# Kernel tuning notes

Hardware: AMD Instinct MI355X
Metric: run time of the kernel (lower is better)

The kernel has to match this reference:

```python
import jax, jax.numpy as jnp
import numpy as np

B, L, C, P, LEVEL, K = 32, 1024, 128, 96, 3, 5
N_NODES = 2 ** (LEVEL + 1) - 1  # 15 CIL blocks in the tree (preorder: node, even-subtree, odd-subtree)
SQRT2 = np.float32(np.sqrt(2.0))


def haar_last(x):
    # Haar wavelet transform along last axis (power-of-2 length), iterative form of the torch recursion:
    # result = [h_final, g_deepest, ..., g_first]
    outs = []
    h = x
    while h.shape[-1] > 1:
        e, o = h[..., ::2], h[..., 1::2]
        outs.append((e - o) / SQRT2)
        h = (e + o) / SQRT2
    return jnp.concatenate([h] + outs[::-1], axis=-1)


def conv1d(x, w, b):
    # x: [B, C, L], w: [O, I, K], b: [O]
    y = jax.lax.conv_general_dilated(x, w, (1,), 'VALID', dimension_numbers=('NCH', 'OIH', 'NCH'))
    return y + b[None, :, None]


def causal_conv_block(x, w1, b1, w2, b2):
    # ReplicationPad1d((K-1, K-1)) -> Conv1d(K) -> LeakyReLU(0.01) -> Conv1d(K) -> Tanh; length preserved
    xp = jnp.pad(x, ((0, 0), (0, 0), (K - 1, K - 1)), mode='edge')
    y = conv1d(xp, w1, b1)
    y = jnp.where(y > 0, y, 0.01 * y)
    return jnp.tanh(conv1d(y, w2, b2))


def cil_block(x, bw1, bb1, bw2, bb2):
    # x: [B, L, C]; bw*: [4, C, C, K] ordered (modules_even, modules_odd, interactor_even, interactor_odd)
    xe = x[:, ::2].transpose(0, 2, 1)   # [B, C, L/2]
    xo = x[:, 1::2].transpose(0, 2, 1)
    ccb = lambda i, z: causal_conv_block(z, bw1[i], bb1[i], bw2[i], bb2[i])
    xet = xe * jnp.exp(ccb(0, xo))
    xot = xo * jnp.exp(ccb(1, xe))
    xeu = xet + ccb(2, xot)
    xou = xot - ccb(3, xet)
    return xeu.transpose(0, 2, 1), xou.transpose(0, 2, 1)


def zip_up(e, o):
    # interleave even/odd halves along the time axis (equal lengths since L is a power of 2)
    b, l, c = e.shape
    return jnp.stack([e, o], axis=2).reshape(b, 2 * l, c)


def _forward(x_enc, mask, fc1_w, fc2_w, ln_g, ln_b, w1, b1, w2, b2, proj_w):
    denom = jnp.sum((mask == 1).astype(x_enc.dtype), axis=1)                 # [B, C]
    means = jax.lax.stop_gradient(jnp.sum(x_enc, axis=1) / denom)[:, None]   # [B, 1, C] (detached)
    x = x_enc - means
    x = jnp.where(mask == 0, 0.0, x)
    stdev = jax.lax.stop_gradient(jnp.sqrt(jnp.sum(x * x, axis=1) / denom + 1e-5))[:, None]
    x = x / stdev
    # haar channel gating block (per-channel haar over time, FC gate, LayerNorm over L)
    freq = haar_last(x.transpose(0, 2, 1))                                   # [B, C, L]
    lr = jax.nn.sigmoid(jax.nn.relu(freq @ fc1_w.T) @ fc2_w.T)               # [B, C, L]
    mu = lr.mean(-1, keepdims=True)
    var = ((lr - mu) ** 2).mean(-1, keepdims=True)                           # biased, as torch LayerNorm
    lr = (lr - mu) / jnp.sqrt(var + 1e-6) * ln_g + ln_b
    x = x * lr.transpose(0, 2, 1)
    # sinusoidal position encoding (pe_hidden_size == C, even)
    num_ts = C // 2
    inc = np.float32(np.log(10000.0) / max(num_ts - 1, 1))
    inv = jnp.exp(jnp.arange(num_ts, dtype=jnp.float32) * -inc)
    st = jnp.arange(L, dtype=jnp.float32)[:, None] * inv[None, :]
    pe = jnp.concatenate([jnp.sin(st), jnp.cos(st)], axis=1)[None]           # [1, L, C]
    x = x + pe
    # recursive CILN tree; node params indexed in call order (node, even-subtree, odd-subtree)
    counter = [0]
    def tree(z, level):
        i = counter[0]; counter[0] += 1
        e, o = cil_block(z, w1[i], b1[i], w2[i], b2[i])
        if level == 0:
            return zip_up(e, o)
        return zip_up(tree(e, level - 1), tree(o, level - 1))
    dec = tree(x, LEVEL) + x
    dec = jnp.einsum('pl,blc->bpc', proj_w, dec)                             # Conv1d(L, L+P, k=1, bias=False) over time dim
    dec = dec * stdev + means
    # forward(): cat(zeros_like(x_enc), dec)[:, -P:, :3] == dec[:, -P:, :3]
    return dec[:, -P:, :3]


def setup_inputs():
    key = jax.random.key(0)
    ks = jax.random.split(key, 8)
    s = 0.05
    return {
        'x_enc': jax.random.normal(ks[0], (B, L, C), jnp.float32),
        'mask': jnp.ones((B, L, C), jnp.float32),
        'fc1_w': jax.random.normal(ks[1], (2 * L, L), jnp.float32) * s,
        'fc2_w': jax.random.normal(ks[2], (L, 2 * L), jnp.float32) * s,
        'ln_g': jnp.ones((L,), jnp.float32),
        'ln_b': jnp.zeros((L,), jnp.float32),
        'w1': jax.random.normal(ks[3], (N_NODES, 4, C, C, K), jnp.float32) * s,
        'b1': jax.random.normal(ks[4], (N_NODES, 4, C), jnp.float32) * s,
        'w2': jax.random.normal(ks[5], (N_NODES, 4, C, C, K), jnp.float32) * s,
        'b2': jax.random.normal(ks[6], (N_NODES, 4, C), jnp.float32) * s,
        'proj_w': jax.random.normal(ks[7], (L + P, L), jnp.float32) * s,
    }


def reference(x_enc, mask, fc1_w, fc2_w, ln_g, ln_b, w1, b1, w2, b2, proj_w):
    return _forward(x_enc, mask, fc1_w, fc2_w, ln_g, ln_b, w1, b1, w2, b2, proj_w)
```

## Files before the change

### kernel.cpp

```cpp
#include <hip/hip_runtime.h>

namespace {

constexpr int NB = 32, NL = 1024, NC = 128, NP = 96, KW = 5;
constexpr float INV_SQRT2 = 0.70710678118654752440f;
constexpr size_t SEG = (size_t)NB * NC;
constexpr int CT = 64;

typedef unsigned short u16;
typedef __attribute__((ext_vector_type(4))) u16 u16x4;
typedef __attribute__((ext_vector_type(8))) u16 u16x8;
typedef __attribute__((ext_vector_type(8))) short short8;
typedef __attribute__((ext_vector_type(4))) float f32x4;

__device__ inline u16 f2bf(float f) {
  unsigned u = __float_as_uint(f);
  u += 0x7fff + ((u >> 16) & 1);
  return (u16)(u >> 16);
}

__device__ inline float ftanh(float x) {
  float e = __expf(2.f * x);
  return 1.f - 2.f / (e + 1.f);
}

__device__ __forceinline__ void glds16(const void* g, void* l) {
  __builtin_amdgcn_global_load_lds(
      (const __attribute__((address_space(1))) unsigned*)g,
      (__attribute__((address_space(3))) unsigned*)l, 16, 0, 0);
}

__global__ void stats1(const float* __restrict__ x, const float* __restrict__ mask,
                       float* __restrict__ part) {
  int b = blockIdx.x, s = blockIdx.y;
  int tid = threadIdx.x;
  int c = tid & 127, lh = tid >> 7;
  const float* xb = x + (size_t)b * NL * NC;
  const float* mb = mask + (size_t)b * NL * NC;
  float s_all = 0.f, d1 = 0.f, sm = 0.f, sm2 = 0.f, cnz = 0.f;
#pragma unroll 4
  for (int i = 0; i < 32; ++i) {
    int l = s * 64 + lh + 2 * i;
    float v = xb[(size_t)l * NC + c];
    float m = mb[(size_t)l * NC + c];
    s_all += v;
    d1 += (m == 1.f) ? 1.f : 0.f;
    bool nz = (m != 0.f);
    float vm = nz ? v : 0.f;
    sm += vm;
    sm2 += vm * v;
    cnz += nz ? 1.f : 0.f;
  }
  __shared__ float red[5][256];
  red[0][tid] = s_all; red[1][tid] = d1; red[2][tid] = sm;
  red[3][tid] = sm2;   red[4][tid] = cnz;
  __syncthreads();
  if (lh == 0) {
    float* pp = part + ((size_t)(b * 16 + s) * 5) * NC + c;
#pragma unroll
    for (int q = 0; q < 5; ++q) pp[q * NC] = red[q][c] + red[q][c + 128];
  }
}

__global__ void stats2(const float* __restrict__ part, float* __restrict__ means,
                       float* __restrict__ stdev) {
  int b = blockIdx.x, c = threadIdx.x;
  float s_all = 0.f, d1 = 0.f, sm = 0.f, sm2 = 0.f, cnz = 0.f;
  for (int s = 0; s < 16; ++s) {
    const float* pp = part + ((size_t)(b * 16 + s) * 5) * NC + c;
    s_all += pp[0];
    d1    += pp[NC];
    sm    += pp[2 * NC];
    sm2   += pp[3 * NC];
    cnz   += pp[4 * NC];
  }
  float mn = s_all / d1;
  float varsum = sm2 - 2.f * mn * sm + mn * mn * cnz;
  means[b * NC + c] = mn;
  stdev[b * NC + c] = sqrtf(varsum / d1 + 1e-5f);
}

__global__ void norm_transpose(const float* __restrict__ x, const float* __restrict__ mask,
                               const float* __restrict__ means, const float* __restrict__ stdev,
                               float* __restrict__ xt) {
  __shared__ float tile[32][33];
  int b = blockIdx.x;
  int l0 = blockIdx.y * 32;
  int c0 = blockIdx.z * 32;
  int tx = threadIdx.x;
  int ty = threadIdx.y;
  for (int i = ty; i < 32; i += 8) {
    int l = l0 + i, c = c0 + tx;
    float v = x[((size_t)b * NL + l) * NC + c];
    float m = mask[((size_t)b * NL + l) * NC + c];
    float val = (m == 0.f) ? 0.f : (v - means[b * NC + c]);
    tile[i][tx] = val / stdev[b * NC + c];
  }
  __syncthreads();
  for (int i = ty; i < 32; i += 8) {
    xt[((size_t)b * NC + c0 + i) * NL + l0 + tx] = tile[tx][i];
  }
}

__global__ void haar_kernel(const float* __restrict__ xt, u16* __restrict__ freqb) {
  int row = blockIdx.x;
  __shared__ float h[1024], t2[512];
  const float* src = xt + (size_t)row * NL;
  u16* dst = freqb + (size_t)row * NL;
  for (int i = threadIdx.x; i < 1024; i += 256) h[i] = src[i];
  __syncthreads();
  int n = 1024;
  while (n > 1) {
    int half = n >> 1;
    for (int i = threadIdx.x; i < half; i += 256) {
      float e = h[2 * i], o = h[2 * i + 1];
      dst[half + i] = f2bf((e - o) * INV_SQRT2);
      t2[i] = (e + o) * INV_SQRT2;
    }
    __syncthreads();
    for (int i = threadIdx.x; i < half; i += 256) h[i] = t2[i];
    __syncthreads();
    n = half;
  }
  if (threadIdx.x == 0) dst[0] = f2bf(h[0]);
}

__global__ void cvt2(const float* __restrict__ in1, const float* __restrict__ in2,
                     u16* __restrict__ o1, u16* __restrict__ o2, int n4) {
  int i = blockIdx.x * 256 + threadIdx.x;
  const float* in = (i < n4) ? in1 : in2;
  u16* op = (i < n4) ? o1 : o2;
  int j = (i < n4) ? i : i - n4;
  if (j < n4) {
    const float4 v = *reinterpret_cast<const float4*>(in + (size_t)j * 4);
    u16x4 o;
    o.x = f2bf(v.x); o.y = f2bf(v.y); o.z = f2bf(v.z); o.w = f2bf(v.w);
    *reinterpret_cast<u16x4*>(op + (size_t)j * 4) = o;
  }
}

__global__ void pack2(const float* __restrict__ w1, const float* __restrict__ w2,
                      u16* __restrict__ wp1, u16* __restrict__ wp2) {
  int idx = blockIdx.x * 256 + threadIdx.x;
  const int NW = 60 * 128 * 128;
  const float* w = (idx < NW) ? w1 : w2;
  u16* wp = (idx < NW) ? wp1 : wp2;
  int j = (idx < NW) ? idx : idx - NW;
  if (j < NW) {
    int ci = j & 127;
    int co = (j >> 7) & 127;
    int n = j >> 14;
    const float* src = w + (size_t)j * 5;
    size_t base = (size_t)n * (5 * 128 * 128) + (size_t)co * 128 + ci;
#pragma unroll
    for (int k = 0; k < 5; ++k)
      wp[base + (size_t)k * 16384] = f2bf(src[k]);
  }
}

__global__ __launch_bounds__(256) void gemm_n128(const u16* __restrict__ A,
                                                 const u16* __restrict__ Bw,
                                                 u16* __restrict__ Cb,
                                                 int M, int N, int K, int CM, int CN) {
  __shared__ __align__(16) char sAB[256 * 128];
  int GX = gridDim.x;
  int h = blockIdx.y * GX + blockIdx.x;
  int xcd = h & 7, loc = h >> 3;
  int lm = loc / CN, ln = loc - lm * CN;
  int cnch = GX / CN;
  int m0 = ((xcd / cnch) * CM + lm) * 128;
  int n0 = ((xcd % cnch) * CN + ln) * 128;
  int tid = threadIdx.x;
  int lane = tid & 63, wv = tid >> 6;
  int wm = (wv >> 1) * 64, wn = (wv & 1) * 64;
  int lg = lane >> 4, l15 = lane & 15;

  const u16* srcb[8];
  int swo[8];
#pragma unroll
  for (int pass = 0; pass < 8; ++pass) {
    int o = pass * 4096 + tid * 16;
    int cb = o & 127;
    int row;
    if (pass < 4) {
      row = o >> 7;
      srcb[pass] = A + (size_t)(m0 + row) * K + (cb >> 1);
    } else {
      int rb = (o - 16384) >> 7;
      row = 128 + rb;
      srcb[pass] = Bw + (size_t)(n0 + rb) * K + (cb >> 1);
    }
    swo[pass] = row * 128 + (cb ^ ((row & 7) << 4));
  }

  f32x4 zero = {0.f, 0.f, 0.f, 0.f};
  f32x4 acc[4][4];
#pragma unroll
  for (int i = 0; i < 4; ++i)
#pragma unroll
    for (int j = 0; j < 4; ++j) acc[i][j] = zero;

  u16x8 st[8];
#pragma unroll
  for (int p = 0; p < 8; ++p) st[p] = *(const u16x8*)(srcb[p]);

  for (int k0 = 0; k0 < K; k0 += 64) {
    __syncthreads();
#pragma unroll
    for (int p = 0; p < 8; ++p) *(u16x8*)(sAB + swo[p]) = st[p];
    __syncthreads();
    if (k0 + 64 < K) {
#pragma unroll
      for (int p = 0; p < 8; ++p) st[p] = *(const u16x8*)(srcb[p] + k0 + 64);
    }
#pragma unroll
    for (int ks = 0; ks < 2; ++ks) {
      int kb = ks * 64 + lg * 16;
      short8 a[4], bbf[4];
#pragma unroll
      for (int mt = 0; mt < 4; ++mt) {
        int rr = wm + mt * 16 + l15;
        a[mt] = *(const short8*)(sAB + rr * 128 + (kb ^ ((rr & 7) << 4)));
      }
#pragma unroll
      for (int nt = 0; nt < 4; ++nt) {
        int rr = 128 + wn + nt * 16 + l15;
        bbf[nt] = *(const short8*)(sAB + rr * 128 + (kb ^ ((rr & 7) << 4)));
      }
#pragma unroll
      for (int mt = 0; mt < 4; ++mt)
#pragma unroll
        for (int nt = 0; nt < 4; ++nt)
          acc[mt][nt] = __builtin_amdgcn_mfma_f32_16x16x32_bf16(a[mt], bbf[nt], acc[mt][nt], 0, 0, 0);
    }
  }
#pragma unroll
  for (int mt = 0; mt < 4; ++mt)
#pragma unroll
    for (int nt = 0; nt < 4; ++nt)
#pragma unroll
      for (int r = 0; r < 4; ++r) {
        int row = m0 + wm + mt * 16 + lg * 4 + r;
        int col = n0 + wn + nt * 16 + l15;
        float v = acc[mt][nt][r];
        v = v > 0.f ? v : 0.f;
        Cb[(size_t)row * N + col] = f2bf(v);
      }
}

__global__ __launch_bounds__(256) void gemm_mfma(const u16* __restrict__ A,
                                                 const u16* __restrict__ Bw,
                                                 float* __restrict__ Cf,
                                                 int M, int N, int K, int CM, int CN) {
  __shared__ __align__(16) char sAB[(128 + 64) * 128];
  int GX = gridDim.x;
  int h = blockIdx.y * GX + blockIdx.x;
  int xcd = h & 7, loc = h >> 3;
  int lm = loc / CN, ln = loc - lm * CN;
  int cnch = GX / CN;
  int m0 = ((xcd / cnch) * CM + lm) * 128;
  int n0 = ((xcd % cnch) * CN + ln) * 64;
  int tid = threadIdx.x;
  int lane = tid & 63, wv = tid >> 6;
  int wm = (wv >> 1) * 64, wn = (wv & 1) * 32;
  int lg = lane >> 4, l15 = lane & 15;

  const u16* srcb[6];
  int swo[6];
#pragma unroll
  for (int pass = 0; pass < 6; ++pass) {
    int o = pass * 4096 + tid * 16;
    int cb = o & 127;
    int row;
    if (pass < 4) {
      row = o >> 7;
      srcb[pass] = A + (size_t)(m0 + row) * K + (cb >> 1);
    } else {
      int rb = (o - 16384) >> 7;
      row = 128 + rb;
      srcb[pass] = Bw + (size_t)(n0 + rb) * K + (cb >> 1);
    }
    swo[pass] = row * 128 + (cb ^ ((row & 7) << 4));
  }

  f32x4 zero = {0.f, 0.f, 0.f, 0.f};
  f32x4 acc[4][2];
#pragma unroll
  for (int i = 0; i < 4; ++i)
#pragma unroll
    for (int j = 0; j < 2; ++j) acc[i][j] = zero;

  u16x8 st[6];
#pragma unroll
  for (int p = 0; p < 6; ++p) st[p] = *(const u16x8*)(srcb[p]);

  for (int k0 = 0; k0 < K; k0 += 64) {
    __syncthreads();
#pragma unroll
    for (int p = 0; p < 6; ++p) *(u16x8*)(sAB + swo[p]) = st[p];
    __syncthreads();
    if (k0 + 64 < K) {
#pragma unroll
      for (int p = 0; p < 6; ++p) st[p] = *(const u16x8*)(srcb[p] + k0 + 64);
    }
#pragma unroll
    for (int ks = 0; ks < 2; ++ks) {
      int kb = ks * 64 + lg * 16;
      short8 a[4], bbf[2];
#pragma unroll
      for (int mt = 0; mt < 4; ++mt) {
        int rr = wm + mt * 16 + l15;
        a[mt] = *(const short8*)(sAB + rr * 128 + (kb ^ ((rr & 7) << 4)));
      }
#pragma unroll
      for (int nt = 0; nt < 2; ++nt) {
        int rr = 128 + wn + nt * 16 + l15;
        bbf[nt] = *(const short8*)(sAB + rr * 128 + (kb ^ ((rr & 7) << 4)));
      }
#pragma unroll
      for (int mt = 0; mt < 4; ++mt)
#pragma unroll
        for (int nt = 0; nt < 2; ++nt)
          acc[mt][nt] = __builtin_amdgcn_mfma_f32_16x16x32_bf16(a[mt], bbf[nt], acc[mt][nt], 0, 0, 0);
    }
  }
#pragma unroll
  for (int mt = 0; mt < 4; ++mt)
#pragma unroll
    for (int nt = 0; nt < 2; ++nt)
#pragma unroll
      for (int r = 0; r < 4; ++r) {
        int row = m0 + wm + mt * 16 + lg * 4 + r;
        int col = n0 + wn + nt * 16 + l15;
        Cf[(size_t)row * N + col] = 1.f / (1.f + __expf(-acc[mt][nt][r]));
      }
}

__global__ void ln_combine(const float* __restrict__ lr, float* __restrict__ xt,
                           const float* __restrict__ g, const float* __restrict__ bta) {
  int row = blockIdx.x;
  int c = row & 127;
  const float* p = lr + (size_t)row * 1024;
  int tid = threadIdx.x;
  float v[4];
#pragma unroll
  for (int i = 0; i < 4; ++i) v[i] = p[tid + 256 * i];
  __shared__ float red[256];
  red[tid] = v[0] + v[1] + v[2] + v[3];
  __syncthreads();
  for (int off = 128; off > 0; off >>= 1) {
    if (tid < off) red[tid] += red[tid + off];
    __syncthreads();
  }
  float mu = red[0] * (1.f / 1024.f);
  __syncthreads();
  float sq = 0.f;
#pragma unroll
  for (int i = 0; i < 4; ++i) { float d = v[i] - mu; sq += d * d; }
  red[tid] = sq;
  __syncthreads();
  for (int off = 128; off > 0; off >>= 1) {
    if (tid < off) red[tid] += red[tid + off];
    __syncthreads();
  }
  float rs = rsqrtf(red[0] * (1.f / 1024.f) + 1e-6f);
  int t = c & 63;
  float inv = __expf(-0.14619589f * (float)t);
  float* xr = xt + (size_t)row * 1024;
#pragma unroll
  for (int i = 0; i < 4; ++i) {
    int l = tid + 256 * i;
    float lrv = (v[i] - mu) * rs * g[l] + bta[l];
    float st = (float)l * inv;
    float pe = (c < 64) ? sinf(st) : cosf(st);
    xr[l] = xr[l] * lrv + pe;
  }
}

__device__ __forceinline__ void stage_w(const u16* W, char* buf, int wv, int lane, int s) {
  int k = s >> 2, ci0 = (s & 3) * 32;
#pragma unroll
  for (int i = 0; i < 2; ++i) {
    int off = i * 1024 + lane * 16;
    int wl = off >> 7;
    int wpos = off & 127;
    int u = wpos ^ ((wl & 7) << 4);
    int co = wv * 32 + wl * 2 + (u >> 6);
    int ci = ci0 + ((u & 63) >> 1);
    glds16(W + (((size_t)(k * 128 + co)) << 7) + ci, buf + wv * 2048 + i * 1024);
  }
}

template <int VAR>
__global__ __launch_bounds__(256) void ccb_fused(
    const float* __restrict__ inF, float* __restrict__ outF,
    const u16* __restrict__ wp1, const u16* __restrict__ wp2,
    const float* __restrict__ b1, const float* __restrict__ b2,
    int d, int Tn) {
  __shared__ __align__(16) char sdat[84 * 256];
  __shared__ __align__(16) char smid[80 * 256];
  __shared__ __align__(16) char wbuf[4][8192];
  int gx = gridDim.x, gy = gridDim.y;
  int total = gx * gy * gridDim.z;
  int hidx = (blockIdx.z * gy + blockIdx.y) * gx + blockIdx.x;
  int lidx = (hidx & 7) * (total >> 3) + (hidx >> 3);
  int b = lidx % gx;
  int rest = lidx / gx;
  int ty = rest % gy;
  int z = rest / gy;
  int p = z >> 1, g = z & 1;
  int node = 0;
  for (int i2 = d - 1; i2 >= 0; --i2) {
    int bit = (p >> i2) & 1;
    int dd = d - 1 - i2;
    node += 1 + bit * ((1 << (3 - dd)) - 1);
  }
  int t0 = CT * ty;
  int tid = threadIdx.x;
  int wq = tid >> 6;
  int lane = tid & 63, wv = wq;
  int lg = lane >> 4, l15 = lane & 15;

  int widx = node * 4 + VAR * 2 + g;
  const u16* W1 = wp1 + (size_t)widx * (5 * 128 * 128);
  const u16* W2 = wp2 + (size_t)widx * (5 * 128 * 128);
  const float* B1 = b1 + (size_t)widx * 128;
  const float* B2 = b2 + (size_t)widx * 128;
  f32x4 bv1[2], bv2[2];
#pragma unroll
  for (int mt = 0; mt < 2; ++mt) {
    bv1[mt] = *(const f32x4*)(B1 + wv * 32 + mt * 16 + lg * 4);
    bv2[mt] = *(const f32x4*)(B2 + wv * 32 + mt * 16 + lg * 4);
  }

  {
    int i = tid & 63;
#pragma unroll
    for (int rep = 0; rep < 2; ++rep) {
      int ii = i + rep * 64;
      if (ii < 84) {
        int sw0 = (ii & 15) << 4;
        int tt = t0 - 8 + ii;
        tt = tt < 0 ? 0 : (tt >= Tn ? Tn - 1 : tt);
        if (VAR == 0) {
          const float* rp = inF + ((size_t)p * SEG + (size_t)b * NC) * (size_t)(2 * Tn) +
                            2 * tt + (1 - g);
#pragma unroll
          for (int pp = 0; pp < 16; ++pp) {
            int pr = wq * 16 + pp;
            float v0 = rp[(size_t)(2 * pr) * (2 * Tn)];
            float v1 = rp[(size_t)(2 * pr + 1) * (2 * Tn)];
            unsigned pk = (unsigned)f2bf(v0) | ((unsigned)f2bf(v1) << 16);
            *(unsigned*)(sdat + ii * 256 + ((4 * pr) ^ sw0)) = pk;
          }
        } else {
          const float* sp = inF + ((size_t)(p * 2 + (g ? 0 : 1)) * SEG + (size_t)b * NC) * Tn + tt;
#pragma unroll
          for (int pp = 0; pp < 16; ++pp) {
            int pr = wq * 16 + pp;
            unsigned pk = (unsigned)f2bf(sp[(size_t)(2 * pr) * Tn]) |
                          ((unsigned)f2bf(sp[(size_t)(2 * pr + 1) * Tn]) << 16);
            *(unsigned*)(sdat + ii * 256 + ((4 * pr) ^ sw0)) = pk;
          }
        }
      }
    }
  }
  stage_w(W1, wbuf[0], wv, lane, 0);
  stage_w(W1, wbuf[1], wv, lane, 1);
  stage_w(W1, wbuf[2], wv, lane, 2);
  stage_w(W1, wbuf[3], wv, lane, 3);
  __syncthreads();

  int co_base = wv * 32 + lg * 4;

  f32x4 acc1[2][5];
#pragma unroll
  for (int mt = 0; mt < 2; ++mt)
#pragma unroll
    for (int nt = 0; nt < 5; ++nt) acc1[mt][nt] = bv1[mt];

#pragma unroll
  for (int s = 0; s < 20; ++s) {
    asm volatile("s_waitcnt vmcnt(6)" ::: "memory");
    __builtin_amdgcn_sched_barrier(0);
    const char* wb = wbuf[s & 3];
    short8 a[2];
#pragma unroll
    for (int mt = 0; mt < 2; ++mt) {
      int co = wv * 32 + mt * 16 + l15;
      int wrow = co >> 1;
      a[mt] = *(const short8*)(wb + wrow * 128 +
                               ((((co & 1) << 6) | (lg << 4)) ^ ((wrow & 7) << 4)));
    }
    int cbyte = 2 * ((s & 3) * 32 + lg * 8);
    int k = s >> 2;
#pragma unroll
    for (int nt = 0; nt < 5; ++nt) {
      int i = nt * 16 + l15 + k;
      short8 bb = *(const short8*)(sdat + i * 256 + (cbyte ^ ((i & 15) << 4)));
#pragma unroll
      for (int mt = 0; mt < 2; ++mt)
        acc1[mt][nt] = __builtin_amdgcn_mfma_f32_16x16x32_bf16(a[mt], bb, acc1[mt][nt], 0, 0, 0);
    }
    {
      asm volatile("s_waitcnt lgkmcnt(0)" ::: "memory");
      __builtin_amdgcn_sched_barrier(0);
      int gs = s + 4;
      if (gs < 20) stage_w(W1, wbuf[s & 3], wv, lane, gs);
      else         stage_w(W2, wbuf[s & 3], wv, lane, gs - 20);
    }
  }

#pragma unroll
  for (int mt = 0; mt < 2; ++mt)
#pragma unroll
    for (int nt = 0; nt < 5; ++nt) {
      int j = nt * 16 + l15;
      int co0 = co_base + mt * 16;
      u16x4 m;
#pragma unroll
      for (int r = 0; r < 4; ++r) {
        float v = acc1[mt][nt][r];
        v = v > 0.f ? v : 0.01f * v;
        m[r] = f2bf(v);
      }
      *(u16x4*)(smid + j * 256 + ((2 * co0) ^ ((j & 15) << 4))) = m;
    }
  __syncthreads();

  f32x4 acc2[2][4];
#pragma unroll
  for (int mt = 0; mt < 2; ++mt)
#pragma unroll
    for (int nt = 0; nt < 4; ++nt) acc2[mt][nt] = bv2[mt];

#pragma unroll
  for (int sp = 0; sp < 20; ++sp) {
    if (sp == 19)      asm volatile("s_waitcnt vmcnt(0)" ::: "memory");
    else if (sp == 18) asm volatile("s_waitcnt vmcnt(2)" ::: "memory");
    else if (sp == 17) asm volatile("s_waitcnt vmcnt(4)" ::: "memory");
    else               asm volatile("s_waitcnt vmcnt(6)" ::: "memory");
    __builtin_amdgcn_sched_barrier(0);
    const char* wb = wbuf[sp & 3];
    short8 a[2];
#pragma unroll
    for (int mt = 0; mt < 2; ++mt) {
      int co = wv * 32 + mt * 16 + l15;
      int wrow = co >> 1;
      a[mt] = *(const short8*)(wb + wrow * 128 +
                               ((((co & 1) << 6) | (lg << 4)) ^ ((wrow & 7) << 4)));
    }
    int cbyte = 2 * ((sp & 3) * 32 + lg * 8);
    int k = sp >> 2;
#pragma unroll
    for (int nt = 0; nt < 4; ++nt) {
      int i = nt * 16 + l15 + k + 4;
      short8 bb = *(const short8*)(smid + i * 256 + (cbyte ^ ((i & 15) << 4)));
#pragma unroll
      for (int mt = 0; mt < 2; ++mt)
        acc2[mt][nt] = __builtin_amdgcn_mfma_f32_16x16x32_bf16(a[mt], bb, acc2[mt][nt], 0, 0, 0);
    }
    if (sp + 4 < 20) {
      asm volatile("s_waitcnt lgkmcnt(0)" ::: "memory");
      __builtin_amdgcn_sched_barrier(0);
      stage_w(W2, wbuf[sp & 3], wv, lane, sp + 4);
    }
  }

  if (VAR == 0) {
    const float* par = inF + ((size_t)p * SEG + (size_t)b * NC) * (size_t)(2 * Tn);
    float* xo_ = outF + ((size_t)(p * 2 + g) * SEG + (size_t)b * NC) * Tn;
#pragma unroll
    for (int mt = 0; mt < 2; ++mt)
#pragma unroll
      for (int nt = 0; nt < 4; ++nt) {
        int t = t0 + nt * 16 + l15;
#pragma unroll
        for (int r = 0; r < 4; ++r) {
          int co = co_base + mt * 16 + r;
          float xv = par[(size_t)co * (2 * Tn) + 2 * t + g];
          xo_[(size_t)co * Tn + t] = xv * __expf(ftanh(acc2[mt][nt][r]));
        }
      }
  } else {
    const float* xf = inF + ((size_t)(p * 2 + g) * SEG + (size_t)b * NC) * Tn;
    float* ch = outF + ((size_t)(2 * p + g) * SEG + (size_t)b * NC) * Tn;
#pragma unroll
    for (int mt = 0; mt < 2; ++mt)
#pragma unroll
      for (int nt = 0; nt < 4; ++nt) {
        int t = t0 + nt * 16 + l15;
#pragma unroll
        for (int r = 0; r < 4; ++r) {
          int co = co_base + mt * 16 + r;
          float cv = ftanh(acc2[mt][nt][r]);
          float base = xf[(size_t)co * Tn + t];
          ch[(size_t)co * Tn + t] = g ? (base - cv) : (base + cv);
        }
      }
  }
}

__global__ void final_kernel(const float* __restrict__ dect, const float* __restrict__ xt,
                             const float* __restrict__ projw, const float* __restrict__ means,
                             const float* __restrict__ stdev, float* __restrict__ out) {
  int b = blockIdx.x, p = blockIdx.y;
  int tid = threadIdx.x;
  const float* w = projw + (size_t)(1024 + p) * 1024;
  const float* x0 = xt + (size_t)b * NC * NL;
  float a[3] = {0.f, 0.f, 0.f};
  for (int l = tid; l < 1024; l += 256) {
    float wv = w[l];
    int rl = l & 7;
    int pb = ((rl & 1) << 2) | (rl & 2) | (rl >> 2);
    int br = (l >> 3) & 1;
    int t = l >> 4;
    const float* dl = dect + ((size_t)(2 * pb + br) * NB + b) * NC * 64 + t;
#pragma unroll
    for (int cc = 0; cc < 3; ++cc)
      a[cc] += wv * (dl[(size_t)cc * 64] + x0[(size_t)cc * NL + l]);
  }
  __shared__ float red[3][256];
  for (int cc = 0; cc < 3; ++cc) red[cc][tid] = a[cc];
  __syncthreads();
  for (int off = 128; off > 0; off >>= 1) {
    if (tid < off) {
      red[0][tid] += red[0][tid + off];
      red[1][tid] += red[1][tid + off];
      red[2][tid] += red[2][tid + off];
    }
    __syncthreads();
  }
  if (tid < 3) {
    out[((size_t)b * NP + p) * 3 + tid] = red[tid][0] * stdev[b * NC + tid] + means[b * NC + tid];
  }
}

}

extern "C" void kernel_launch(void* const* d_in, const int* in_sizes, int n_in,
                              void* d_out, int out_size, void* d_ws, size_t ws_size,
                              hipStream_t stream) {
  (void)in_sizes; (void)n_in; (void)out_size; (void)ws_size;
  const float* x_enc = (const float*)d_in[0];
  const float* mask  = (const float*)d_in[1];
  const float* fc1_w = (const float*)d_in[2];
  const float* fc2_w = (const float*)d_in[3];
  const float* ln_g  = (const float*)d_in[4];
  const float* ln_b  = (const float*)d_in[5];
  const float* w1    = (const float*)d_in[6];
  const float* b1    = (const float*)d_in[7];
  const float* w2    = (const float*)d_in[8];
  const float* b2    = (const float*)d_in[9];
  const float* projw = (const float*)d_in[10];
  float* out = (float*)d_out;
  float* ws = (float*)d_ws;

  float* means = ws + 0;
  float* stdev = ws + 4096;
  float* x_t   = ws + 8192;
  float* freq  = ws + 4202496;
  float* IN1   = ws + 8396800;
  float* IN2   = ws + 12591104;
  float* xeof  = ws + 16785408;
  float* wp1f  = ws + 20979712;
  float* wp2f  = ws + 23437312;
  float* dect = IN1;
  float* stats_part = wp2f;
  u16* freq_bf = (u16*)xeof;
  u16* hid_bf  = (u16*)IN1;
  u16* fc1w_bf = (u16*)IN2;
  u16* fc2w_bf = (u16*)(IN2 + 1048576);
  u16* wp1 = (u16*)wp1f;
  u16* wp2 = (u16*)wp2f;

  stats1<<<dim3(NB, 16), 256, 0, stream>>>(x_enc, mask, stats_part);
  stats2<<<NB, 128, 0, stream>>>(stats_part, means, stdev);
  norm_transpose<<<dim3(NB, NL / 32, NC / 32), dim3(32, 8), 0, stream>>>(x_enc, mask, means, stdev, x_t);
  haar_kernel<<<NB * NC, 256, 0, stream>>>(x_t, freq_bf);

  cvt2<<<4096, 256, 0, stream>>>(fc1_w, fc2_w, fc1w_bf, fc2w_bf, 524288);
  pack2<<<7680, 256, 0, stream>>>(w1, w2, wp1, wp2);

  gemm_n128<<<dim3(16, 32), 256, 0, stream>>>(freq_bf, fc1w_bf, hid_bf,
                                              4096, 2048, 1024, 8, 8);
  gemm_mfma<<<dim3(16, 32), 256, 0, stream>>>(hid_bf, fc2w_bf, freq,
                                              4096, 1024, 2048, 8, 8);

  ln_combine<<<4096, 256, 0, stream>>>(freq, x_t, ln_g, ln_b);

  float* dbuf[5] = {x_t, IN1, IN2, freq, IN1};
  for (int d = 0; d < 4; ++d) {
    int Tn = 512 >> d;
    int nsub = 1 << d;
    dim3 grd(NB, Tn / CT, 2 * nsub);
    ccb_fused<0><<<grd, 256, 0, stream>>>(dbuf[d], xeof, wp1, wp2, b1, b2, d, Tn);
    ccb_fused<1><<<grd, 256, 0, stream>>>(xeof, dbuf[d + 1], wp1, wp2, b1, b2, d, Tn);
  }

  final_kernel<<<dim3(NB, NP), 256, 0, stream>>>(dect, x_t, projw, means, stdev, out);
}
```

Before: 328.0 us.

## Load conv weight fragments directly into registers instead of staging through LDS

```diff
diff --git a/kernel.cpp b/kernel.cpp
--- a/kernel.cpp
+++ b/kernel.cpp
@@ -22,12 +22,6 @@
 __device__ inline float ftanh(float x) {
   float e = __expf(2.f * x);
   return 1.f - 2.f / (e + 1.f);
-}
-
-__device__ __forceinline__ void glds16(const void* g, void* l) {
-  __builtin_amdgcn_global_load_lds(
-      (const __attribute__((address_space(1))) unsigned*)g,
-      (__attribute__((address_space(3))) unsigned*)l, 16, 0, 0);
 }
 
 __global__ void stats1(const float* __restrict__ x, const float* __restrict__ mask,
@@ -377,20 +371,6 @@
   }
 }
 
-__device__ __forceinline__ void stage_w(const u16* W, char* buf, int wv, int lane, int s) {
-  int k = s >> 2, ci0 = (s & 3) * 32;
-#pragma unroll
-  for (int i = 0; i < 2; ++i) {
-    int off = i * 1024 + lane * 16;
-    int wl = off >> 7;
-    int wpos = off & 127;
-    int u = wpos ^ ((wl & 7) << 4);
-    int co = wv * 32 + wl * 2 + (u >> 6);
-    int ci = ci0 + ((u & 63) >> 1);
-    glds16(W + (((size_t)(k * 128 + co)) << 7) + ci, buf + wv * 2048 + i * 1024);
-  }
-}
-
 template <int VAR>
 __global__ __launch_bounds__(256) void ccb_fused(
     const float* __restrict__ inF, float* __restrict__ outF,
@@ -399,7 +379,6 @@
     int d, int Tn) {
   __shared__ __align__(16) char sdat[84 * 256];
   __shared__ __align__(16) char smid[80 * 256];
-  __shared__ __align__(16) char wbuf[4][8192];
   int gx = gridDim.x, gy = gridDim.y;
   int total = gx * gy * gridDim.z;
   int hidx = (blockIdx.z * gy + blockIdx.y) * gx + blockIdx.x;
@@ -433,6 +412,18 @@
     bv2[mt] = *(const f32x4*)(B2 + wv * 32 + mt * 16 + lg * 4);
   }
 
+  int co_l[2] = {wv * 32 + l15, wv * 32 + 16 + l15};
+  int ciL = lg * 8;
+
+  u16x8 wreg[4][2];
+#pragma unroll
+  for (int s = 0; s < 4; ++s) {
+    int k = s >> 2, ci0 = (s & 3) * 32 + ciL;
+#pragma unroll
+    for (int mt = 0; mt < 2; ++mt)
+      wreg[s][mt] = *(const u16x8*)(W1 + (((size_t)(k * 128 + co_l[mt])) << 7) + ci0);
+  }
+
   {
     int i = tid & 63;
 #pragma unroll
@@ -466,10 +457,6 @@
       }
     }
   }
-  stage_w(W1, wbuf[0], wv, lane, 0);
-  stage_w(W1, wbuf[1], wv, lane, 1);
-  stage_w(W1, wbuf[2], wv, lane, 2);
-  stage_w(W1, wbuf[3], wv, lane, 3);
   __syncthreads();
 
   int co_base = wv * 32 + lg * 4;
@@ -482,33 +469,25 @@
 
 #pragma unroll
   for (int s = 0; s < 20; ++s) {
-    asm volatile("s_waitcnt vmcnt(6)" ::: "memory");
-    __builtin_amdgcn_sched_barrier(0);
-    const char* wb = wbuf[s & 3];
-    short8 a[2];
-#pragma unroll
-    for (int mt = 0; mt < 2; ++mt) {
-      int co = wv * 32 + mt * 16 + l15;
-      int wrow = co >> 1;
-      a[mt] = *(const short8*)(wb + wrow * 128 +
-                               ((((co & 1) << 6) | (lg << 4)) ^ ((wrow & 7) << 4)));
-    }
+    short8 a0 = (short8)wreg[s & 3][0];
+    short8 a1 = (short8)wreg[s & 3][1];
     int cbyte = 2 * ((s & 3) * 32 + lg * 8);
     int k = s >> 2;
 #pragma unroll
     for (int nt = 0; nt < 5; ++nt) {
       int i = nt * 16 + l15 + k;
       short8 bb = *(const short8*)(sdat + i * 256 + (cbyte ^ ((i & 15) << 4)));
+      acc1[0][nt] = __builtin_amdgcn_mfma_f32_16x16x32_bf16(a0, bb, acc1[0][nt], 0, 0, 0);
+      acc1[1][nt] = __builtin_amdgcn_mfma_f32_16x16x32_bf16(a1, bb, acc1[1][nt], 0, 0, 0);
+    }
+    {
+      int gs = s + 4;
+      const u16* W = (gs < 20) ? W1 : W2;
+      int ls = (gs < 20) ? gs : gs - 20;
+      int kk = ls >> 2, ci0 = (ls & 3) * 32 + ciL;
 #pragma unroll
       for (int mt = 0; mt < 2; ++mt)
-        acc1[mt][nt] = __builtin_amdgcn_mfma_f32_16x16x32_bf16(a[mt], bb, acc1[mt][nt], 0, 0, 0);
-    }
-    {
-      asm volatile("s_waitcnt lgkmcnt(0)" ::: "memory");
-      __builtin_amdgcn_sched_barrier(0);
-      int gs = s + 4;
-      if (gs < 20) stage_w(W1, wbuf[s & 3], wv, lane, gs);
-      else         stage_w(W2, wbuf[s & 3], wv, lane, gs - 20);
+        wreg[s & 3][mt] = *(const u16x8*)(W + (((size_t)(kk * 128 + co_l[mt])) << 7) + ci0);
     }
   }
 
@@ -537,34 +516,23 @@
 
 #pragma unroll
   for (int sp = 0; sp < 20; ++sp) {
-    if (sp == 19)      asm volatile("s_waitcnt vmcnt(0)" ::: "memory");
-    else if (sp == 18) asm volatile("s_waitcnt vmcnt(2)" ::: "memory");
-    else if (sp == 17) asm volatile("s_waitcnt vmcnt(4)" ::: "memory");
-    else               asm volatile("s_waitcnt vmcnt(6)" ::: "memory");
-    __builtin_amdgcn_sched_barrier(0);
-    const char* wb = wbuf[sp & 3];
-    short8 a[2];
-#pragma unroll
-    for (int mt = 0; mt < 2; ++mt) {
-      int co = wv * 32 + mt * 16 + l15;
-      int wrow = co >> 1;
-      a[mt] = *(const short8*)(wb + wrow * 128 +
-                               ((((co & 1) << 6) | (lg << 4)) ^ ((wrow & 7) << 4)));
-    }
+    short8 a0 = (short8)wreg[sp & 3][0];
+    short8 a1 = (short8)wreg[sp & 3][1];
     int cbyte = 2 * ((sp & 3) * 32 + lg * 8);
     int k = sp >> 2;
 #pragma unroll
     for (int nt = 0; nt < 4; ++nt) {
       int i = nt * 16 + l15 + k + 4;
       short8 bb = *(const short8*)(smid + i * 256 + (cbyte ^ ((i & 15) << 4)));
+      acc2[0][nt] = __builtin_amdgcn_mfma_f32_16x16x32_bf16(a0, bb, acc2[0][nt], 0, 0, 0);
+      acc2[1][nt] = __builtin_amdgcn_mfma_f32_16x16x32_bf16(a1, bb, acc2[1][nt], 0, 0, 0);
+    }
+    if (sp + 4 < 20) {
+      int ls = sp + 4;
+      int kk = ls >> 2, ci0 = (ls & 3) * 32 + ciL;
 #pragma unroll
       for (int mt = 0; mt < 2; ++mt)
-        acc2[mt][nt] = __builtin_amdgcn_mfma_f32_16x16x32_bf16(a[mt], bb, acc2[mt][nt], 0, 0, 0);
-    }
-    if (sp + 4 < 20) {
-      asm volatile("s_waitcnt lgkmcnt(0)" ::: "memory");
-      __builtin_amdgcn_sched_barrier(0);
-      stage_w(W2, wbuf[sp & 3], wv, lane, sp + 4);
+        wreg[sp & 3][mt] = *(const u16x8*)(W2 + (((size_t)(kk * 128 + co_l[mt])) << 7) + ci0);
     }
   }
 
```

Measured after the change: 392.7 us. 1.2x slower.
